# Optimization experiments

Hardware: AMD Instinct MI355X
Metric: run time of the kernel (lower is better)

Reference implementation:

```python
import jax, jax.numpy as jnp
import numpy as np

DT = 1e-3
TAU_SYN_INV = 200.0      # 1/5e-3
TAU_MEM_INV = 100.0      # 1/1e-2
TAU_ADAPT_INV = 1.0 / 700.0
V_TH = 1.0
BETA = 1.8
ALPHA = 100.0            # SuperSpike surrogate slope
SEQ_LEN = 40
SCALE = 50.0


@jax.custom_vjp
def superspike(x):
    return (x > 0).astype(x.dtype)

def _ss_fwd(x):
    return (x > 0).astype(x.dtype), x

def _ss_bwd(x, g):
    # SuperSpike surrogate gradient: 1 / (alpha*|x| + 1)^2
    return (g / (ALPHA * jnp.abs(x) + 1.0) ** 2,)

superspike.defvjp(_ss_fwd, _ss_bwd)


def lif_encode(current):
    """Constant-current LIF encoder: current [B,F] -> spikes [T,B,F]."""
    def step(v, _):
        v = v + DT * TAU_MEM_INV * (-v + current)   # v_leak = 0
        z = superspike(v - V_TH)
        v = (1.0 - z) * v                           # reset to v_reset = 0
        return v, z
    _, spikes = jax.lax.scan(step, jnp.zeros_like(current), None, length=SEQ_LEN)
    return spikes


def setup_inputs() -> dict:
    key = jax.random.key(0)
    kx, k1, k2, k3, kd = jax.random.split(key, 5)
    B, S, H, O = 16384, 4, 128, 2
    x = jax.random.normal(kx, (B, S), jnp.float32)
    w_in = jax.random.normal(k1, (H, 2 * S), jnp.float32) * np.sqrt(2.0 / H).astype(np.float32)
    w_rec = jax.random.normal(k2, (H, H), jnp.float32) * np.sqrt(2.0 / H).astype(np.float32)
    w_out = jax.random.normal(k3, (O, H), jnp.float32) * np.sqrt(2.0 / O).astype(np.float32)
    keep = jax.random.bernoulli(kd, 0.5, (SEQ_LEN, B, H))
    drop_mask = keep.astype(jnp.float32) * 2.0      # inverted dropout, p=0.5
    return {"x": x, "w_in": w_in, "w_rec": w_rec, "w_out": w_out,
            "drop_mask": drop_mask}


def reference(x, w_in, w_rec, w_out, drop_mask):
    # Encode state into pos/neg spike trains: [T, B, 2*S]
    x_pos = lif_encode(jax.nn.relu(SCALE * x))
    x_neg = lif_encode(jax.nn.relu(-SCALE * x))
    inp = jnp.concatenate([x_pos, x_neg], axis=2)

    B = x.shape[0]
    H = w_in.shape[0]
    O = w_out.shape[0]
    zH = jnp.zeros((B, H), x.dtype)
    zO = jnp.zeros((B, O), x.dtype)
    carry0 = (zH, zH, zH, zH, zO, zO)  # (z, v, i, b, v_out, i_out)

    def step(carry, xs):
        z, v, i, b, vo, io = carry
        x_t, m_t = xs
        # --- LSNN cell (norse lsnn_step) ---
        v_dec = v + DT * TAU_MEM_INV * (-v + i)        # v_leak = 0
        i_dec = i - DT * TAU_SYN_INV * i
        b_dec = b + DT * TAU_ADAPT_INV * (V_TH - b)
        z_new = superspike(v_dec - b_dec)
        v_new = (1.0 - z_new) * v_dec                  # v_reset = 0
        i_new = i_dec + x_t @ w_in.T + z @ w_rec.T
        b_new = b_dec + z_new * (TAU_ADAPT_INV * BETA)
        # dropout (training mode, p=0.5, precomputed inverted mask)
        z_d = z_new * m_t
        # --- LI readout (norse li_step) ---
        vo_new = vo + DT * TAU_MEM_INV * (-vo + io)
        io_new = io - DT * TAU_SYN_INV * io + z_d @ w_out.T
        return (z_new, v_new, i_new, b_new, vo_new, io_new), vo_new

    _, voltages = jax.lax.scan(step, carry0, (inp, drop_mask))  # [T, B, O]
    m = jnp.max(voltages, axis=0)
    return jax.nn.softmax(m, axis=1)
```

## Files before the change

### kernel.cpp

```cpp
#include <hip/hip_runtime.h>
#include <math.h>
#include <string.h>

#define TSTEPS 40
#define BTOT   16384
#define HDIM   128
#define BT     16
#define NWAVE  8

typedef __attribute__((ext_vector_type(8))) short bf16x8;
typedef __attribute__((ext_vector_type(4))) float f32x4;

__device__ __forceinline__ short f2bf(float f) {
    unsigned int u;
    memcpy(&u, &f, 4);
    unsigned int lsb = (u >> 16) & 1u;
    u += 0x7fffu + lsb;
    return (short)(u >> 16);
}
__device__ __forceinline__ float bf2f(short s) {
    unsigned int u = ((unsigned int)(unsigned short)s) << 16;
    float f;
    memcpy(&f, &u, 4);
    return f;
}

__global__ __launch_bounds__(512, 2)
void lsnn_mfma(const float* __restrict__ x,
               const float* __restrict__ w_in,
               const float* __restrict__ w_rec,
               const float* __restrict__ w_out,
               const float* __restrict__ dm,
               float* __restrict__ out)
{
    __shared__ short zbuf[BT][136];
    __shared__ short xt[BT][8];
    __shared__ float red[NWAVE][BT][2];

    const int tid   = threadIdx.x;
    const int l     = tid & 63;
    const int wv    = tid >> 6;
    const int li    = l & 15;
    const int q     = l >> 4;
    const int bbase = blockIdx.x * BT;
    const int hcol  = wv * 16 + li;

    bf16x8 wB[4][3];
    #pragma unroll
    for (int kt = 0; kt < 4; ++kt) {
        const float* src = w_rec + hcol * HDIM + kt * 32 + q * 8;
        #pragma unroll
        for (int i = 0; i < 8; ++i) {
            float w0 = src[i];
            short h0 = f2bf(w0); float r1 = w0 - bf2f(h0);
            short h1 = f2bf(r1); float r2 = r1 - bf2f(h1);
            short h2 = f2bf(r2);
            wB[kt][0][i] = h0; wB[kt][1][i] = h1; wB[kt][2][i] = h2;
        }
    }
    bf16x8 wiB[3];
    #pragma unroll
    for (int p = 0; p < 3; ++p)
        #pragma unroll
        for (int i = 0; i < 8; ++i) wiB[p][i] = 0;
    if (q == 0) {
        const float* src = w_in + hcol * 8;
        #pragma unroll
        for (int i = 0; i < 8; ++i) {
            float w0 = src[i];
            short h0 = f2bf(w0); float r1 = w0 - bf2f(h0);
            short h1 = f2bf(r1); float r2 = r1 - bf2f(h1);
            short h2 = f2bf(r2);
            wiB[0][i] = h0; wiB[1][i] = h1; wiB[2][i] = h2;
        }
    }
    const float wo0 = w_out[hcol];
    const float wo1 = w_out[HDIM + hcol];

    f32x4 v  = {0.f, 0.f, 0.f, 0.f};
    f32x4 cu = {0.f, 0.f, 0.f, 0.f};
    f32x4 ba = {0.f, 0.f, 0.f, 0.f};

    float ve = 0.f, ce = 0.f;
    const int g = wv * 64 + l;
    if (wv < 2) {
        int er = g >> 3, ech = g & 7;
        float xv = 50.f * x[(bbase + er) * 4 + (ech & 3)];
        ce = (ech < 4) ? fmaxf(xv, 0.f) : fmaxf(-xv, 0.f);
    }
    float vo = 0.f, io = 0.f, mx = 0.f;

    const float KA = 1.4285714285714286e-06f;
    const float KB = 2.5714285714285714e-03f;

    for (int idx = tid; idx < BT * 136; idx += 512) ((short*)zbuf)[idx] = 0;
    __syncthreads();

    float mr[4];
    {
        const float* dmt = dm + (size_t)bbase * HDIM;
        #pragma unroll
        for (int r = 0; r < 4; ++r) mr[r] = dmt[(q * 4 + r) * HDIM + hcol];
    }

    for (int t = 0; t < TSTEPS; ++t) {
        float sp = 0.f;
        if (wv < 2) {
            float vv = ve + 0.1f * (ce - ve);
            sp = (vv - 1.0f > 0.f) ? 1.f : 0.f;
            ve = (1.f - sp) * vv;
        }
        bf16x8 zA[4];
        #pragma unroll
        for (int kt = 0; kt < 4; ++kt)
            zA[kt] = *reinterpret_cast<const bf16x8*>(&zbuf[li][kt * 32 + q * 8]);
        if (wv < 2) xt[g >> 3][g & 7] = (sp > 0.5f) ? (short)0x3F80 : (short)0;
        __syncthreads();

        float mrn[4];
        {
            int tn = (t + 1 < TSTEPS) ? t + 1 : TSTEPS - 1;
            const float* dmn = dm + ((size_t)tn * BTOT + bbase) * HDIM;
            #pragma unroll
            for (int r = 0; r < 4; ++r) mrn[r] = dmn[(q * 4 + r) * HDIM + hcol];
        }
        bf16x8 xA;
        #pragma unroll
        for (int i = 0; i < 8; ++i) xA[i] = 0;
        if (q == 0) xA = *reinterpret_cast<const bf16x8*>(&xt[li][0]);

        f32x4 acc = {0.f, 0.f, 0.f, 0.f};
        #pragma unroll
        for (int p = 0; p < 3; ++p) {
            acc = __builtin_amdgcn_mfma_f32_16x16x32_bf16(xA, wiB[p], acc, 0, 0, 0);
            #pragma unroll
            for (int kt = 0; kt < 4; ++kt)
                acc = __builtin_amdgcn_mfma_f32_16x16x32_bf16(zA[kt], wB[kt][p], acc, 0, 0, 0);
        }

        float p0r[4], p1r[4];
        #pragma unroll
        for (int r = 0; r < 4; ++r) {
            float vd = v[r] + 0.1f * (cu[r] - v[r]);
            float id = cu[r] - 0.2f * cu[r];
            float bd = ba[r] + KA * (1.0f - ba[r]);
            float z  = (vd - bd > 0.f) ? 1.f : 0.f;
            v[r]  = (1.f - z) * vd;
            ba[r] = bd + z * KB;
            cu[r] = id + acc[r];
            float zd = z * mr[r];
            p0r[r] = zd * wo0;
            p1r[r] = zd * wo1;
            zbuf[q * 4 + r][hcol] = (z > 0.5f) ? (short)0x3F80 : (short)0;
        }
        #pragma unroll
        for (int s = 1; s < 16; s <<= 1) {
            #pragma unroll
            for (int r = 0; r < 4; ++r) {
                p0r[r] += __shfl_xor(p0r[r], s);
                p1r[r] += __shfl_xor(p1r[r], s);
            }
        }
        if (li == 0) {
            #pragma unroll
            for (int r = 0; r < 4; ++r) {
                red[wv][q * 4 + r][0] = p0r[r];
                red[wv][q * 4 + r][1] = p1r[r];
            }
        }
        __syncthreads();

        if (wv == 0 && l < 32) {
            int row = l >> 1, o = l & 1;
            float s = 0.f;
            #pragma unroll
            for (int w = 0; w < NWAVE; ++w) s += red[w][row][o];
            float von = vo + 0.1f * (io - vo);
            io = io - 0.2f * io + s;
            vo = von;
            mx = fmaxf(mx, vo);
        }
        #pragma unroll
        for (int r = 0; r < 4; ++r) mr[r] = mrn[r];
    }

    if (wv == 0 && l < 32) {
        int row = l >> 1, o = l & 1;
        float other = __shfl_xor(mx, 1);
        float mmax  = fmaxf(mx, other);
        float e  = expf(mx - mmax);
        float eo = expf(other - mmax);
        out[(size_t)(bbase + row) * 2 + o] = e / (e + eo);
    }
}

extern "C" void kernel_launch(void* const* d_in, const int* in_sizes, int n_in,
                              void* d_out, int out_size, void* d_ws, size_t ws_size,
                              hipStream_t stream) {
    const float* x     = (const float*)d_in[0];
    const float* w_in  = (const float*)d_in[1];
    const float* w_rec = (const float*)d_in[2];
    const float* w_out = (const float*)d_in[3];
    const float* dmask = (const float*)d_in[4];
    float* outp = (float*)d_out;

    lsnn_mfma<<<BTOT / BT, 512, 0, stream>>>(x, w_in, w_rec, w_out, dmask, outp);
}
```

Before: 564.8 us.

## Process 64 batch rows per block to reuse register-resident weights across row tiles

```diff
diff --git a/kernel.cpp b/kernel.cpp
--- a/kernel.cpp
+++ b/kernel.cpp
@@ -5,8 +5,9 @@
 #define TSTEPS 40
 #define BTOT   16384
 #define HDIM   128
-#define BT     16
+#define BT     64
 #define NWAVE  8
+#define ZSTR   136
 
 typedef __attribute__((ext_vector_type(8))) short bf16x8;
 typedef __attribute__((ext_vector_type(4))) float f32x4;
@@ -26,14 +27,14 @@
 }
 
 __global__ __launch_bounds__(512, 2)
-void lsnn_mfma(const float* __restrict__ x,
-               const float* __restrict__ w_in,
-               const float* __restrict__ w_rec,
-               const float* __restrict__ w_out,
-               const float* __restrict__ dm,
-               float* __restrict__ out)
+void lsnn_mfma64(const float* __restrict__ x,
+                 const float* __restrict__ w_in,
+                 const float* __restrict__ w_rec,
+                 const float* __restrict__ w_out,
+                 const float* __restrict__ dm,
+                 float* __restrict__ out)
 {
-    __shared__ short zbuf[BT][136];
+    __shared__ short zbuf[BT][ZSTR];
     __shared__ short xt[BT][8];
     __shared__ float red[NWAVE][BT][2];
 
@@ -77,101 +78,124 @@
     const float wo0 = w_out[hcol];
     const float wo1 = w_out[HDIM + hcol];
 
-    f32x4 v  = {0.f, 0.f, 0.f, 0.f};
-    f32x4 cu = {0.f, 0.f, 0.f, 0.f};
-    f32x4 ba = {0.f, 0.f, 0.f, 0.f};
-
-    float ve = 0.f, ce = 0.f;
-    const int g = wv * 64 + l;
-    if (wv < 2) {
-        int er = g >> 3, ech = g & 7;
+    f32x4 v[4], cu[4], ba[4];
+    #pragma unroll
+    for (int rt = 0; rt < 4; ++rt) {
+        v[rt]  = (f32x4){0.f, 0.f, 0.f, 0.f};
+        cu[rt] = (f32x4){0.f, 0.f, 0.f, 0.f};
+        ba[rt] = (f32x4){0.f, 0.f, 0.f, 0.f};
+    }
+
+    const int er = tid >> 3, ech = tid & 7;
+    float ve = 0.f, ce;
+    {
         float xv = 50.f * x[(bbase + er) * 4 + (ech & 3)];
         ce = (ech < 4) ? fmaxf(xv, 0.f) : fmaxf(-xv, 0.f);
     }
+
     float vo = 0.f, io = 0.f, mx = 0.f;
 
     const float KA = 1.4285714285714286e-06f;
     const float KB = 2.5714285714285714e-03f;
 
-    for (int idx = tid; idx < BT * 136; idx += 512) ((short*)zbuf)[idx] = 0;
+    for (int idx = tid; idx < BT * ZSTR; idx += 512) ((short*)zbuf)[idx] = 0;
     __syncthreads();
 
-    float mr[4];
+    float mr[4][4];
     {
         const float* dmt = dm + (size_t)bbase * HDIM;
         #pragma unroll
-        for (int r = 0; r < 4; ++r) mr[r] = dmt[(q * 4 + r) * HDIM + hcol];
+        for (int rt = 0; rt < 4; ++rt)
+            #pragma unroll
+            for (int r = 0; r < 4; ++r)
+                mr[rt][r] = dmt[(rt * 16 + q * 4 + r) * HDIM + hcol];
     }
 
     for (int t = 0; t < TSTEPS; ++t) {
-        float sp = 0.f;
-        if (wv < 2) {
+        {
             float vv = ve + 0.1f * (ce - ve);
-            sp = (vv - 1.0f > 0.f) ? 1.f : 0.f;
+            float sp = (vv - 1.0f > 0.f) ? 1.f : 0.f;
             ve = (1.f - sp) * vv;
-        }
-        bf16x8 zA[4];
-        #pragma unroll
-        for (int kt = 0; kt < 4; ++kt)
-            zA[kt] = *reinterpret_cast<const bf16x8*>(&zbuf[li][kt * 32 + q * 8]);
-        if (wv < 2) xt[g >> 3][g & 7] = (sp > 0.5f) ? (short)0x3F80 : (short)0;
+            xt[er][ech] = (sp > 0.5f) ? (short)0x3F80 : (short)0;
+        }
+
+        f32x4 acc[4];
+        #pragma unroll
+        for (int rt = 0; rt < 4; ++rt) {
+            bf16x8 zA[4];
+            #pragma unroll
+            for (int kt = 0; kt < 4; ++kt)
+                zA[kt] = *reinterpret_cast<const bf16x8*>(&zbuf[rt * 16 + li][kt * 32 + q * 8]);
+            f32x4 a = {0.f, 0.f, 0.f, 0.f};
+            #pragma unroll
+            for (int p = 0; p < 3; ++p)
+                #pragma unroll
+                for (int kt = 0; kt < 4; ++kt)
+                    a = __builtin_amdgcn_mfma_f32_16x16x32_bf16(zA[kt], wB[kt][p], a, 0, 0, 0);
+            acc[rt] = a;
+        }
         __syncthreads();
 
-        float mrn[4];
+        float mrn[4][4];
         {
             int tn = (t + 1 < TSTEPS) ? t + 1 : TSTEPS - 1;
             const float* dmn = dm + ((size_t)tn * BTOT + bbase) * HDIM;
             #pragma unroll
-            for (int r = 0; r < 4; ++r) mrn[r] = dmn[(q * 4 + r) * HDIM + hcol];
-        }
-        bf16x8 xA;
-        #pragma unroll
-        for (int i = 0; i < 8; ++i) xA[i] = 0;
-        if (q == 0) xA = *reinterpret_cast<const bf16x8*>(&xt[li][0]);
-
-        f32x4 acc = {0.f, 0.f, 0.f, 0.f};
-        #pragma unroll
-        for (int p = 0; p < 3; ++p) {
-            acc = __builtin_amdgcn_mfma_f32_16x16x32_bf16(xA, wiB[p], acc, 0, 0, 0);
-            #pragma unroll
-            for (int kt = 0; kt < 4; ++kt)
-                acc = __builtin_amdgcn_mfma_f32_16x16x32_bf16(zA[kt], wB[kt][p], acc, 0, 0, 0);
-        }
-
-        float p0r[4], p1r[4];
-        #pragma unroll
-        for (int r = 0; r < 4; ++r) {
-            float vd = v[r] + 0.1f * (cu[r] - v[r]);
-            float id = cu[r] - 0.2f * cu[r];
-            float bd = ba[r] + KA * (1.0f - ba[r]);
-            float z  = (vd - bd > 0.f) ? 1.f : 0.f;
-            v[r]  = (1.f - z) * vd;
-            ba[r] = bd + z * KB;
-            cu[r] = id + acc[r];
-            float zd = z * mr[r];
-            p0r[r] = zd * wo0;
-            p1r[r] = zd * wo1;
-            zbuf[q * 4 + r][hcol] = (z > 0.5f) ? (short)0x3F80 : (short)0;
-        }
-        #pragma unroll
-        for (int s = 1; s < 16; s <<= 1) {
+            for (int rt = 0; rt < 4; ++rt)
+                #pragma unroll
+                for (int r = 0; r < 4; ++r)
+                    mrn[rt][r] = dmn[(rt * 16 + q * 4 + r) * HDIM + hcol];
+        }
+
+        #pragma unroll
+        for (int rt = 0; rt < 4; ++rt) {
+            bf16x8 xA;
+            #pragma unroll
+            for (int i = 0; i < 8; ++i) xA[i] = 0;
+            if (q == 0) xA = *reinterpret_cast<const bf16x8*>(&xt[rt * 16 + li][0]);
+            #pragma unroll
+            for (int p = 0; p < 3; ++p)
+                acc[rt] = __builtin_amdgcn_mfma_f32_16x16x32_bf16(xA, wiB[p], acc[rt], 0, 0, 0);
+        }
+
+        #pragma unroll
+        for (int rt = 0; rt < 4; ++rt) {
+            float p0r[4], p1r[4];
             #pragma unroll
             for (int r = 0; r < 4; ++r) {
-                p0r[r] += __shfl_xor(p0r[r], s);
-                p1r[r] += __shfl_xor(p1r[r], s);
+                float vd = v[rt][r] + 0.1f * (cu[rt][r] - v[rt][r]);
+                float id = cu[rt][r] - 0.2f * cu[rt][r];
+                float bd = ba[rt][r] + KA * (1.0f - ba[rt][r]);
+                float z  = (vd - bd > 0.f) ? 1.f : 0.f;
+                v[rt][r]  = (1.f - z) * vd;
+                ba[rt][r] = bd + z * KB;
+                cu[rt][r] = id + acc[rt][r];
+                zbuf[rt * 16 + q * 4 + r][hcol] = (z > 0.5f) ? (short)0x3F80 : (short)0;
+                float zd = z * mr[rt][r];
+                p0r[r] = zd * wo0;
+                p1r[r] = zd * wo1;
             }
-        }
-        if (li == 0) {
-            #pragma unroll
-            for (int r = 0; r < 4; ++r) {
-                red[wv][q * 4 + r][0] = p0r[r];
-                red[wv][q * 4 + r][1] = p1r[r];
+            #pragma unroll
+            for (int s = 1; s < 16; s <<= 1) {
+                #pragma unroll
+                for (int r = 0; r < 4; ++r) {
+                    p0r[r] += __shfl_xor(p0r[r], s);
+                    p1r[r] += __shfl_xor(p1r[r], s);
+                }
             }
+            if (li == 0) {
+                #pragma unroll
+                for (int r = 0; r < 4; ++r) {
+                    red[wv][rt * 16 + q * 4 + r][0] = p0r[r];
+                    red[wv][rt * 16 + q * 4 + r][1] = p1r[r];
+                }
+            }
         }
         __syncthreads();
 
-        if (wv == 0 && l < 32) {
-            int row = l >> 1, o = l & 1;
+        if (wv < 2) {
+            int g = wv * 64 + l;
+            int row = g >> 1, o = g & 1;
             float s = 0.f;
             #pragma unroll
             for (int w = 0; w < NWAVE; ++w) s += red[w][row][o];
@@ -181,11 +205,15 @@
             mx = fmaxf(mx, vo);
         }
         #pragma unroll
-        for (int r = 0; r < 4; ++r) mr[r] = mrn[r];
-    }
-
-    if (wv == 0 && l < 32) {
-        int row = l >> 1, o = l & 1;
+        for (int rt = 0; rt < 4; ++rt)
+            #pragma unroll
+            for (int r = 0; r < 4; ++r) mr[rt][r] = mrn[rt][r];
+    }
+
+    if (wv < 2) {
+        int g = wv * 64 + l;
+        int row = g >> 1;
+        int o = g & 1;
         float other = __shfl_xor(mx, 1);
         float mmax  = fmaxf(mx, other);
         float e  = expf(mx - mmax);
@@ -204,5 +232,5 @@
     const float* dmask = (const float*)d_in[4];
     float* outp = (float*)d_out;
 
-    lsnn_mfma<<<BTOT / BT, 512, 0, stream>>>(x, w_in, w_rec, w_out, dmask, outp);
-}
+    lsnn_mfma64<<<BTOT / BT, 512, 0, stream>>>(x, w_in, w_rec, w_out, dmask, outp);
+}
```

Result: faster. 533.6 us (-5.5%).

## Double-buffer spikes and dropout mask in LDS, doubling batch rows per block

Applied to the files above, without the earlier changes.

```diff
diff --git a/kernel.cpp b/kernel.cpp
--- a/kernel.cpp
+++ b/kernel.cpp
@@ -5,37 +5,40 @@
 #define TSTEPS 40
 #define BTOT   16384
 #define HDIM   128
-#define BT     16
+#define BT     32
+#define ZSTR   168
 #define NWAVE  8
 
 typedef __attribute__((ext_vector_type(8))) short bf16x8;
 typedef __attribute__((ext_vector_type(4))) float f32x4;
 
 __device__ __forceinline__ short f2bf(float f) {
-    unsigned int u;
-    memcpy(&u, &f, 4);
-    unsigned int lsb = (u >> 16) & 1u;
-    u += 0x7fffu + lsb;
+    unsigned int u; memcpy(&u, &f, 4);
+    u += 0x7fffu + ((u >> 16) & 1u);
     return (short)(u >> 16);
 }
 __device__ __forceinline__ float bf2f(short s) {
     unsigned int u = ((unsigned int)(unsigned short)s) << 16;
-    float f;
-    memcpy(&f, &u, 4);
+    float f; memcpy(&f, &u, 4);
     return f;
 }
-
-__global__ __launch_bounds__(512, 2)
-void lsnn_mfma(const float* __restrict__ x,
-               const float* __restrict__ w_in,
-               const float* __restrict__ w_rec,
-               const float* __restrict__ w_out,
-               const float* __restrict__ dm,
-               float* __restrict__ out)
+__device__ __forceinline__ void gload_lds16(const float* g, void* lds) {
+    __builtin_amdgcn_global_load_lds(
+        (const __attribute__((address_space(1))) void*)g,
+        (__attribute__((address_space(3))) void*)lds, 16, 0, 0);
+}
+
+__global__ __launch_bounds__(512, 4)
+void lsnn5(const float* __restrict__ x,
+           const float* __restrict__ w_in,
+           const float* __restrict__ w_rec,
+           const float* __restrict__ w_out,
+           const float* __restrict__ dm,
+           float* __restrict__ out)
 {
-    __shared__ short zbuf[BT][136];
-    __shared__ short xt[BT][8];
-    __shared__ float red[NWAVE][BT][2];
+    __shared__ short zbuf[2][BT][ZSTR];
+    __shared__ float dmb[2][BT * HDIM];
+    __shared__ float red[2][NWAVE][BT][2];
 
     const int tid   = threadIdx.x;
     const int l     = tid & 63;
@@ -45,7 +48,7 @@
     const int bbase = blockIdx.x * BT;
     const int hcol  = wv * 16 + li;
 
-    bf16x8 wB[4][3];
+    bf16x8 wB[5][3];
     #pragma unroll
     for (int kt = 0; kt < 4; ++kt) {
         const float* src = w_rec + hcol * HDIM + kt * 32 + q * 8;
@@ -54,15 +57,11 @@
             float w0 = src[i];
             short h0 = f2bf(w0); float r1 = w0 - bf2f(h0);
             short h1 = f2bf(r1); float r2 = r1 - bf2f(h1);
-            short h2 = f2bf(r2);
-            wB[kt][0][i] = h0; wB[kt][1][i] = h1; wB[kt][2][i] = h2;
-        }
-    }
-    bf16x8 wiB[3];
+            wB[kt][0][i] = h0; wB[kt][1][i] = h1; wB[kt][2][i] = f2bf(r2);
+        }
+    }
     #pragma unroll
-    for (int p = 0; p < 3; ++p)
-        #pragma unroll
-        for (int i = 0; i < 8; ++i) wiB[p][i] = 0;
+    for (int i = 0; i < 8; ++i) { wB[4][0][i] = 0; wB[4][1][i] = 0; wB[4][2][i] = 0; }
     if (q == 0) {
         const float* src = w_in + hcol * 8;
         #pragma unroll
@@ -70,122 +69,137 @@
             float w0 = src[i];
             short h0 = f2bf(w0); float r1 = w0 - bf2f(h0);
             short h1 = f2bf(r1); float r2 = r1 - bf2f(h1);
-            short h2 = f2bf(r2);
-            wiB[0][i] = h0; wiB[1][i] = h1; wiB[2][i] = h2;
+            wB[4][0][i] = h0; wB[4][1][i] = h1; wB[4][2][i] = f2bf(r2);
         }
     }
     const float wo0 = w_out[hcol];
     const float wo1 = w_out[HDIM + hcol];
 
-    f32x4 v  = {0.f, 0.f, 0.f, 0.f};
-    f32x4 cu = {0.f, 0.f, 0.f, 0.f};
-    f32x4 ba = {0.f, 0.f, 0.f, 0.f};
+    f32x4 v[2], cu[2], ba[2];
+    #pragma unroll
+    for (int rt = 0; rt < 2; ++rt) {
+        v[rt]  = (f32x4){0.f,0.f,0.f,0.f};
+        cu[rt] = (f32x4){0.f,0.f,0.f,0.f};
+        ba[rt] = (f32x4){0.f,0.f,0.f,0.f};
+    }
 
     float ve = 0.f, ce = 0.f;
-    const int g = wv * 64 + l;
-    if (wv < 2) {
-        int er = g >> 3, ech = g & 7;
-        float xv = 50.f * x[(bbase + er) * 4 + (ech & 3)];
-        ce = (ech < 4) ? fmaxf(xv, 0.f) : fmaxf(-xv, 0.f);
-    }
+    if (tid < 256) {
+        float xv = 50.f * x[(bbase + (tid >> 3)) * 4 + (tid & 3)];
+        ce = ((tid & 7) < 4) ? fmaxf(xv, 0.f) : fmaxf(-xv, 0.f);
+    }
+
     float vo = 0.f, io = 0.f, mx = 0.f;
 
     const float KA = 1.4285714285714286e-06f;
     const float KB = 2.5714285714285714e-03f;
 
-    for (int idx = tid; idx < BT * 136; idx += 512) ((short*)zbuf)[idx] = 0;
+    for (int idx = tid; idx < 2 * BT * ZSTR; idx += 512) ((short*)zbuf)[idx] = 0;
+    for (int idx = tid; idx < NWAVE * BT * 2; idx += 512) ((float*)red)[idx] = 0.f;
     __syncthreads();
 
-    float mr[4];
+    if (tid < 256) {
+        float vv = ve + 0.1f * (ce - ve);
+        float sp = (vv - 1.0f > 0.f) ? 1.f : 0.f;
+        ve = (1.f - sp) * vv;
+        zbuf[0][tid >> 3][128 + (tid & 7)] = (sp > 0.5f) ? (short)0x3F80 : (short)0;
+    }
     {
-        const float* dmt = dm + (size_t)bbase * HDIM;
-        #pragma unroll
-        for (int r = 0; r < 4; ++r) mr[r] = dmt[(q * 4 + r) * HDIM + hcol];
+        const float* g = dm + (size_t)bbase * HDIM;
+        char* lb = (char*)&dmb[0][0];
+        gload_lds16(g + tid * 4, lb + tid * 16);
+        gload_lds16(g + 2048 + tid * 4, lb + 8192 + tid * 16);
     }
 
     for (int t = 0; t < TSTEPS; ++t) {
-        float sp = 0.f;
-        if (wv < 2) {
-            float vv = ve + 0.1f * (ce - ve);
-            sp = (vv - 1.0f > 0.f) ? 1.f : 0.f;
-            ve = (1.f - sp) * vv;
-        }
-        bf16x8 zA[4];
-        #pragma unroll
-        for (int kt = 0; kt < 4; ++kt)
-            zA[kt] = *reinterpret_cast<const bf16x8*>(&zbuf[li][kt * 32 + q * 8]);
-        if (wv < 2) xt[g >> 3][g & 7] = (sp > 0.5f) ? (short)0x3F80 : (short)0;
+        const int p = t & 1;
         __syncthreads();
 
-        float mrn[4];
         {
             int tn = (t + 1 < TSTEPS) ? t + 1 : TSTEPS - 1;
-            const float* dmn = dm + ((size_t)tn * BTOT + bbase) * HDIM;
-            #pragma unroll
-            for (int r = 0; r < 4; ++r) mrn[r] = dmn[(q * 4 + r) * HDIM + hcol];
-        }
-        bf16x8 xA;
-        #pragma unroll
-        for (int i = 0; i < 8; ++i) xA[i] = 0;
-        if (q == 0) xA = *reinterpret_cast<const bf16x8*>(&xt[li][0]);
-
-        f32x4 acc = {0.f, 0.f, 0.f, 0.f};
-        #pragma unroll
-        for (int p = 0; p < 3; ++p) {
-            acc = __builtin_amdgcn_mfma_f32_16x16x32_bf16(xA, wiB[p], acc, 0, 0, 0);
-            #pragma unroll
-            for (int kt = 0; kt < 4; ++kt)
-                acc = __builtin_amdgcn_mfma_f32_16x16x32_bf16(zA[kt], wB[kt][p], acc, 0, 0, 0);
-        }
-
-        float p0r[4], p1r[4];
-        #pragma unroll
-        for (int r = 0; r < 4; ++r) {
-            float vd = v[r] + 0.1f * (cu[r] - v[r]);
-            float id = cu[r] - 0.2f * cu[r];
-            float bd = ba[r] + KA * (1.0f - ba[r]);
-            float z  = (vd - bd > 0.f) ? 1.f : 0.f;
-            v[r]  = (1.f - z) * vd;
-            ba[r] = bd + z * KB;
-            cu[r] = id + acc[r];
-            float zd = z * mr[r];
-            p0r[r] = zd * wo0;
-            p1r[r] = zd * wo1;
-            zbuf[q * 4 + r][hcol] = (z > 0.5f) ? (short)0x3F80 : (short)0;
-        }
-        #pragma unroll
-        for (int s = 1; s < 16; s <<= 1) {
-            #pragma unroll
-            for (int r = 0; r < 4; ++r) {
-                p0r[r] += __shfl_xor(p0r[r], s);
-                p1r[r] += __shfl_xor(p1r[r], s);
-            }
-        }
-        if (li == 0) {
-            #pragma unroll
-            for (int r = 0; r < 4; ++r) {
-                red[wv][q * 4 + r][0] = p0r[r];
-                red[wv][q * 4 + r][1] = p1r[r];
-            }
-        }
-        __syncthreads();
-
-        if (wv == 0 && l < 32) {
+            const float* g = dm + ((size_t)tn * BTOT + bbase) * HDIM;
+            char* lb = (char*)&dmb[1 - p][0];
+            gload_lds16(g + tid * 4, lb + tid * 16);
+            gload_lds16(g + 2048 + tid * 4, lb + 8192 + tid * 16);
+        }
+
+        if (wv == 0) {
             int row = l >> 1, o = l & 1;
             float s = 0.f;
             #pragma unroll
-            for (int w = 0; w < NWAVE; ++w) s += red[w][row][o];
+            for (int w = 0; w < NWAVE; ++w) s += red[p][w][row][o];
             float von = vo + 0.1f * (io - vo);
             io = io - 0.2f * io + s;
             vo = von;
             mx = fmaxf(mx, vo);
         }
-        #pragma unroll
-        for (int r = 0; r < 4; ++r) mr[r] = mrn[r];
-    }
-
-    if (wv == 0 && l < 32) {
+
+        if (tid < 256) {
+            float vv = ve + 0.1f * (ce - ve);
+            float sp = (vv - 1.0f > 0.f) ? 1.f : 0.f;
+            ve = (1.f - sp) * vv;
+            zbuf[1 - p][tid >> 3][128 + (tid & 7)] = (sp > 0.5f) ? (short)0x3F80 : (short)0;
+        }
+
+        f32x4 acc[2];
+        #pragma unroll
+        for (int rt = 0; rt < 2; ++rt) {
+            f32x4 a = {0.f, 0.f, 0.f, 0.f};
+            #pragma unroll
+            for (int kt = 0; kt < 5; ++kt) {
+                bf16x8 zA = *reinterpret_cast<const bf16x8*>(&zbuf[p][rt * 16 + li][kt * 32 + q * 8]);
+                #pragma unroll
+                for (int pp = 0; pp < 3; ++pp)
+                    a = __builtin_amdgcn_mfma_f32_16x16x32_bf16(zA, wB[kt][pp], a, 0, 0, 0);
+            }
+            acc[rt] = a;
+        }
+
+        #pragma unroll
+        for (int rt = 0; rt < 2; ++rt) {
+            float p0r[4], p1r[4];
+            #pragma unroll
+            for (int r = 0; r < 4; ++r) {
+                int row = rt * 16 + q * 4 + r;
+                float vd = v[rt][r] + 0.1f * (cu[rt][r] - v[rt][r]);
+                float id = cu[rt][r] - 0.2f * cu[rt][r];
+                float bd = ba[rt][r] + KA * (1.0f - ba[rt][r]);
+                float z  = (vd - bd > 0.f) ? 1.f : 0.f;
+                v[rt][r]  = (1.f - z) * vd;
+                ba[rt][r] = bd + z * KB;
+                cu[rt][r] = id + acc[rt][r];
+                zbuf[1 - p][row][hcol] = (z > 0.5f) ? (short)0x3F80 : (short)0;
+                float zd = z * dmb[p][row * HDIM + hcol];
+                p0r[r] = zd * wo0;
+                p1r[r] = zd * wo1;
+            }
+            #pragma unroll
+            for (int s = 1; s < 16; s <<= 1) {
+                #pragma unroll
+                for (int r = 0; r < 4; ++r) {
+                    p0r[r] += __shfl_xor(p0r[r], s);
+                    p1r[r] += __shfl_xor(p1r[r], s);
+                }
+            }
+            if (li == 0) {
+                #pragma unroll
+                for (int r = 0; r < 4; ++r) {
+                    red[1 - p][wv][rt * 16 + q * 4 + r][0] = p0r[r];
+                    red[1 - p][wv][rt * 16 + q * 4 + r][1] = p1r[r];
+                }
+            }
+        }
+    }
+
+    __syncthreads();
+    if (wv == 0) {
         int row = l >> 1, o = l & 1;
+        float s = 0.f;
+        #pragma unroll
+        for (int w = 0; w < NWAVE; ++w) s += red[TSTEPS & 1][w][row][o];
+        float von = vo + 0.1f * (io - vo);
+        vo = von;
+        mx = fmaxf(mx, vo);
         float other = __shfl_xor(mx, 1);
         float mmax  = fmaxf(mx, other);
         float e  = expf(mx - mmax);
@@ -204,5 +218,5 @@
     const float* dmask = (const float*)d_in[4];
     float* outp = (float*)d_out;
 
-    lsnn_mfma<<<BTOT / BT, 512, 0, stream>>>(x, w_in, w_rec, w_out, dmask, outp);
-}
+    lsnn5<<<BTOT / BT, 512, 0, stream>>>(x, w_in, w_rec, w_out, dmask, outp);
+}
```

Result: slower. 869.0 us (+53.8%).
